# Performance work log

Hardware: AMD Instinct MI355X
Metric: run time of the kernel (lower is better)

The kernel has to match this reference:

```python
import jax, jax.numpy as jnp
import numpy as np

DX = 64  # state dim
DY = 64  # observation dim
B = 64   # batch of independent series
T = 512  # time_extent


def setup_inputs() -> dict:
    key = jax.random.key(0)
    ks = jax.random.split(key, 9)
    Ix = jnp.eye(DX, dtype=jnp.float32)
    Iy = jnp.eye(DY, dtype=jnp.float32)
    observation = jax.random.normal(ks[0], (T + 1, B, DY), dtype=jnp.float32)
    prior_mean = 0.1 * jax.random.normal(ks[1], (DX,), dtype=jnp.float32)
    prior_chol = 0.3 * Ix + jnp.tril(0.02 * jax.random.normal(ks[2], (DX, DX), dtype=jnp.float32))
    dynamic_weight = 0.9 * Ix + 0.02 * jax.random.normal(ks[3], (DX, DX), dtype=jnp.float32)
    dynamic_bias = 0.01 * jax.random.normal(ks[4], (DX,), dtype=jnp.float32)
    dynamic_chol = 0.3 * Ix + jnp.tril(0.02 * jax.random.normal(ks[5], (DX, DX), dtype=jnp.float32))
    observation_weight = Iy + 0.05 * jax.random.normal(ks[6], (DY, DX), dtype=jnp.float32)
    observation_bias = 0.01 * jax.random.normal(ks[7], (DY,), dtype=jnp.float32)
    observation_chol = 0.3 * Iy + jnp.tril(0.02 * jax.random.normal(ks[8], (DY, DY), dtype=jnp.float32))
    return {
        "time_extent": T,
        "observation": observation,
        "prior_mean": prior_mean,
        "prior_chol": prior_chol,
        "dynamic_weight": dynamic_weight,
        "dynamic_bias": dynamic_bias,
        "dynamic_chol": dynamic_chol,
        "observation_weight": observation_weight,
        "observation_bias": observation_bias,
        "observation_chol": observation_chol,
    }


def reference(time_extent, observation, prior_mean, prior_chol, dynamic_weight,
              dynamic_bias, dynamic_chol, observation_weight, observation_bias,
              observation_chol):
    dtype = observation.dtype
    dx = prior_mean.shape[-1]
    dy = observation.shape[-1]
    b = observation.shape[1]
    half_log_2pi = 0.5 * jnp.log(jnp.asarray(2.0 * np.pi, dtype))

    P0 = prior_chol @ prior_chol.T            # (dx, dx) prior covariance
    Q = dynamic_chol @ dynamic_chol.T         # process noise
    R = observation_chol @ observation_chol.T # observation noise
    F = dynamic_weight
    H = observation_weight
    Ix = jnp.eye(dx, dtype=dtype)

    def log_density(mean, cov, y):
        # mean: (1,dy) or (b,dy); cov: (dy,dy); y: (b,dy)
        res = y - mean
        inv = jnp.linalg.inv(cov)
        pref = -dy * half_log_2pi - 0.5 * jnp.linalg.slogdet(cov)[1]
        return pref - 0.5 * jnp.einsum('bi,ij,bj->b', res, inv, res)

    def bayes_update(mean, P, y):
        # mean: (b,dx) or (1,dx); P: (dx,dx); y: (b,dy)
        CW = P @ H.T                               # (dx, dy)
        S_inv = jnp.linalg.inv(H @ CW + R)         # (dy, dy)
        WIW = H.T @ S_inv @ H                      # (dx, dx)
        post_P = P @ (Ix - WIW @ P)
        post_mean = mean @ (Ix - P @ WIW).T + (y - observation_bias) @ (CW @ S_inv).T
        return post_mean, post_P

    # t = 0: predictive of observation from the prior
    obs_mean0 = prior_mean[None, :] @ H.T + observation_bias  # (1, dy)
    obs_cov0 = H @ P0 @ H.T + R
    ll0 = log_density(obs_mean0, obs_cov0, observation[0])
    m0, P0_post = bayes_update(prior_mean[None, :], P0, observation[0])
    m0 = jnp.broadcast_to(m0, (b, dx))

    def step(carry, y):
        m, P = carry
        pm = m @ F.T + dynamic_bias                # predictive mean (b, dx)
        pP = F @ P @ F.T + Q                       # predictive cov (dx, dx)
        om = pm @ H.T + observation_bias           # obs predictive mean
        oC = H @ pP @ H.T + R
        ll = log_density(om, oC, y)
        nm, nP = bayes_update(pm, pP, y)
        return (nm, nP), (nm, nP, ll)

    (_, _), (ms, Ps, lls) = jax.lax.scan(step, (m0, P0_post), observation[1:])
    posterior_means = jnp.concatenate([m0[None], ms], axis=0)          # (T+1, b, dx)
    covs = jnp.concatenate([P0_post[None], Ps], axis=0)                # (T+1, dx, dx)
    posterior_covariances = jnp.broadcast_to(covs[:, None], (time_extent + 1, b, dx, dx))
    likelihood_factors = jnp.concatenate([ll0[None], lls], axis=0)     # (T+1, b)
    return posterior_means, posterior_covariances, likelihood_factors
```

## Files before the change

kernel.cpp:

```cpp
#include <hip/hip_runtime.h>
#include <math.h>


#define TID ((int)threadIdx.x)
#define LDA 68
#define MAT 4096
#define BSLOT 4096
#define NSLOT 513
#define HEAD 64

#define WS_CSTAGE 0
#define WS_U      (NSLOT*MAT)
#define WS_EB     (WS_U + 9*MAT)
#define WS_CQ     (WS_EB + 4*MAT)
#define WS_CR     (WS_CQ + MAT)
#define WS_CHQ    (WS_CR + MAT)
#define WS_G      (WS_CHQ + MAT)
#define WS_KGT    (WS_G + MAT)
#define WS_HF     (WS_KGT + MAT)
#define WS_P0     (WS_HF + MAT)
#define WS_HP0    (WS_P0 + MAT)
#define WS_BA     (WS_HP0 + MAT)
#define WS_OBHDB  (WS_BA + 64)
#define WS_OM0    (WS_OBHDB + 64)
#define WS_HDB    (WS_OM0 + 64)
#define WS_SG     (WS_HDB + 64)
#define WS_B0     (WS_SG + MAT)
#define WS_B1     (WS_B0 + NSLOT*BSLOT)
#define WS_E0     (WS_B1 + NSLOT*BSLOT)
#define WS_E1     (WS_E0 + NSLOT*BSLOT)
#define WS_PP     (WS_E1 + NSLOT*BSLOT)
#define WS_SSI    (WS_PP + MAT)
#define WS_KST    (WS_SSI + MAT)
#define WS_BASS   (WS_KST + MAT)
#define WS_LDSS   (WS_BASS + 64)
#define WS_MK     (WS_LDSS + 64)

#define OUT_M 0
#define OUT_C 2101248
#define OUT_L 136581120

#define LLC (-58.81206612509905f)


__device__ __forceinline__ void tload(float* dst, const float* __restrict__ g) {
#pragma unroll
  for (int p = TID; p < 1024; p += 256) {
    int m = p >> 4, k4 = (p & 15) << 2;
    float4 v = *(const float4*)(g + m*64 + k4);
    dst[(k4+0)*LDA + m] = v.x;
    dst[(k4+1)*LDA + m] = v.y;
    dst[(k4+2)*LDA + m] = v.z;
    dst[(k4+3)*LDA + m] = v.w;
  }
}

__device__ __forceinline__ void tload_sub(float* dst, const float* __restrict__ g,
                                          const float* __restrict__ vec) {
#pragma unroll
  for (int p = TID; p < 1024; p += 256) {
    int m = p >> 4, k4 = (p & 15) << 2;
    float4 v = *(const float4*)(g + m*64 + k4);
    float4 s = *(const float4*)(vec + k4);
    dst[(k4+0)*LDA + m] = v.x - s.x;
    dst[(k4+1)*LDA + m] = v.y - s.y;
    dst[(k4+2)*LDA + m] = v.z - s.z;
    dst[(k4+3)*LDA + m] = v.w - s.w;
  }
}

__device__ __forceinline__ void pload(float* dst, const float* __restrict__ g) {
#pragma unroll
  for (int p = TID; p < 1024; p += 256) {
    int m = p >> 4, c4 = (p & 15) << 2;
    *(float4*)(dst + m*LDA + c4) = *(const float4*)(g + m*64 + c4);
  }
}

__device__ __forceinline__ void transcopy(float* dst, const float* src) {
#pragma unroll
  for (int p = TID; p < 1024; p += 256) {
    int m = p >> 4, k4 = (p & 15) << 2;
    float4 v = *(const float4*)(src + m*LDA + k4);
    dst[(k4+0)*LDA + m] = v.x;
    dst[(k4+1)*LDA + m] = v.y;
    dst[(k4+2)*LDA + m] = v.z;
    dst[(k4+3)*LDA + m] = v.w;
  }
}

__device__ __forceinline__ void gemm(const float* As, const float* Bs,
                                     float a[4][4], int tr, int tc) {
#pragma unroll
  for (int i = 0; i < 4; ++i)
#pragma unroll
    for (int j = 0; j < 4; ++j) a[i][j] = 0.f;
  const float* ap = As + (tr << 2);
  const float* bp = Bs + (tc << 2);
#pragma unroll 8
  for (int kk = 0; kk < 64; ++kk) {
    float4 av = *(const float4*)ap; ap += LDA;
    float4 bv = *(const float4*)bp; bp += LDA;
    a[0][0] = fmaf(av.x, bv.x, a[0][0]); a[0][1] = fmaf(av.x, bv.y, a[0][1]);
    a[0][2] = fmaf(av.x, bv.z, a[0][2]); a[0][3] = fmaf(av.x, bv.w, a[0][3]);
    a[1][0] = fmaf(av.y, bv.x, a[1][0]); a[1][1] = fmaf(av.y, bv.y, a[1][1]);
    a[1][2] = fmaf(av.y, bv.z, a[1][2]); a[1][3] = fmaf(av.y, bv.w, a[1][3]);
    a[2][0] = fmaf(av.z, bv.x, a[2][0]); a[2][1] = fmaf(av.z, bv.y, a[2][1]);
    a[2][2] = fmaf(av.z, bv.z, a[2][2]); a[2][3] = fmaf(av.z, bv.w, a[2][3]);
    a[3][0] = fmaf(av.w, bv.x, a[3][0]); a[3][1] = fmaf(av.w, bv.y, a[3][1]);
    a[3][2] = fmaf(av.w, bv.z, a[3][2]); a[3][3] = fmaf(av.w, bv.w, a[3][3]);
  }
}

__device__ __forceinline__ void add_g(float a[4][4], const float* __restrict__ g,
                                      int tr, int tc) {
#pragma unroll
  for (int i = 0; i < 4; ++i) {
    float4 v = *(const float4*)(g + (4*tr+i)*64 + 4*tc);
    a[i][0] += v.x; a[i][1] += v.y; a[i][2] += v.z; a[i][3] += v.w;
  }
}

__device__ __forceinline__ void rsub_g(float a[4][4], const float* __restrict__ g,
                                       int tr, int tc) {
#pragma unroll
  for (int i = 0; i < 4; ++i) {
    float4 v = *(const float4*)(g + (4*tr+i)*64 + 4*tc);
    a[i][0] = v.x - a[i][0]; a[i][1] = v.y - a[i][1];
    a[i][2] = v.z - a[i][2]; a[i][3] = v.w - a[i][3];
  }
}

__device__ __forceinline__ void addvec_g(float a[4][4], const float* __restrict__ v,
                                         int tc) {
  float4 s = *(const float4*)(v + 4*tc);
#pragma unroll
  for (int i = 0; i < 4; ++i) {
    a[i][0] += s.x; a[i][1] += s.y; a[i][2] += s.z; a[i][3] += s.w;
  }
}

__device__ __forceinline__ void addI(float a[4][4], int tr, int tc) {
  if (tr == tc) { a[0][0] += 1.f; a[1][1] += 1.f; a[2][2] += 1.f; a[3][3] += 1.f; }
}

__device__ __forceinline__ void gwrite(float* g, float a[4][4], int tr, int tc) {
#pragma unroll
  for (int i = 0; i < 4; ++i)
    *(float4*)(g + (4*tr+i)*64 + 4*tc) = make_float4(a[i][0], a[i][1], a[i][2], a[i][3]);
}

__device__ __forceinline__ void twrite_g(float* g, float a[4][4], int tr, int tc) {
#pragma unroll
  for (int i = 0; i < 4; ++i)
#pragma unroll
    for (int j = 0; j < 4; ++j)
      g[(4*tc+j)*64 + 4*tr+i] = a[i][j];
}

__device__ __forceinline__ void pstore(float* dst, float a[4][4], int tr, int tc) {
#pragma unroll
  for (int i = 0; i < 4; ++i)
    *(float4*)(dst + (4*tr+i)*LDA + 4*tc) = make_float4(a[i][0], a[i][1], a[i][2], a[i][3]);
}

__device__ __forceinline__ void tstore(float* dst, float a[4][4], int tr, int tc) {
#pragma unroll
  for (int i = 0; i < 4; ++i)
#pragma unroll
    for (int j = 0; j < 4; ++j)
      dst[(4*tc+j)*LDA + 4*tr+i] = a[i][j];
}

__device__ __forceinline__ void pwrite_g(float* g, const float* lds) {
#pragma unroll
  for (int p = TID; p < 1024; p += 256) {
    int m = p >> 4, c4 = (p & 15) << 2;
    *(float4*)(g + m*64 + c4) = *(const float4*)(lds + m*LDA + c4);
  }
}

__device__ float gj_inverse2(float* M, float* gjb, int wantLog) {
  const int i = TID >> 2, q = TID & 3;
  float r[16];
  {
    const float* base = M + i*LDA + 16*q;
    float4 v0 = *(const float4*)(base + 0);
    float4 v1 = *(const float4*)(base + 4);
    float4 v2 = *(const float4*)(base + 8);
    float4 v3 = *(const float4*)(base + 12);
    r[0]=v0.x; r[1]=v0.y; r[2]=v0.z; r[3]=v0.w;
    r[4]=v1.x; r[5]=v1.y; r[6]=v1.z; r[7]=v1.w;
    r[8]=v2.x; r[9]=v2.y; r[10]=v2.z; r[11]=v2.w;
    r[12]=v3.x; r[13]=v3.y; r[14]=v3.z; r[15]=v3.w;
  }
  float ld = 0.f;
  float* cb = gjb;
  float* rb = gjb + 128;
#pragma unroll 64
  for (int j = 0; j < 64; ++j) {
    float* cbp = cb + (j & 1) * 64;
    float* rbp = rb + (j & 1) * 64;
    if (q == (j >> 4)) cbp[i] = r[j & 15];
    if (i == j) {
      *(float4*)(rbp + 16*q + 0)  = make_float4(r[0], r[1], r[2], r[3]);
      *(float4*)(rbp + 16*q + 4)  = make_float4(r[4], r[5], r[6], r[7]);
      *(float4*)(rbp + 16*q + 8)  = make_float4(r[8], r[9], r[10], r[11]);
      *(float4*)(rbp + 16*q + 12) = make_float4(r[12], r[13], r[14], r[15]);
    }
    __syncthreads();
    float p = cbp[j];
    float rp = 1.0f / p;
    if (wantLog) ld += logf(p);
    float f = cbp[i];
    float mu = (i == j) ? (rp - 1.0f) : (0.0f - f * rp);
    float4 p0 = *(const float4*)(rbp + 16*q + 0);
    float4 p1 = *(const float4*)(rbp + 16*q + 4);
    float4 p2 = *(const float4*)(rbp + 16*q + 8);
    float4 p3 = *(const float4*)(rbp + 16*q + 12);
    r[0]  = fmaf(mu, p0.x, r[0]);  r[1]  = fmaf(mu, p0.y, r[1]);
    r[2]  = fmaf(mu, p0.z, r[2]);  r[3]  = fmaf(mu, p0.w, r[3]);
    r[4]  = fmaf(mu, p1.x, r[4]);  r[5]  = fmaf(mu, p1.y, r[5]);
    r[6]  = fmaf(mu, p1.z, r[6]);  r[7]  = fmaf(mu, p1.w, r[7]);
    r[8]  = fmaf(mu, p2.x, r[8]);  r[9]  = fmaf(mu, p2.y, r[9]);
    r[10] = fmaf(mu, p2.z, r[10]); r[11] = fmaf(mu, p2.w, r[11]);
    r[12] = fmaf(mu, p3.x, r[12]); r[13] = fmaf(mu, p3.y, r[13]);
    r[14] = fmaf(mu, p3.z, r[14]); r[15] = fmaf(mu, p3.w, r[15]);
    if (q == (j >> 4)) r[j & 15] = (i == j) ? rp : mu;
  }
  {
    float* base = M + i*LDA + 16*q;
    *(float4*)(base + 0)  = make_float4(r[0], r[1], r[2], r[3]);
    *(float4*)(base + 4)  = make_float4(r[4], r[5], r[6], r[7]);
    *(float4*)(base + 8)  = make_float4(r[8], r[9], r[10], r[11]);
    *(float4*)(base + 12) = make_float4(r[12], r[13], r[14], r[15]);
  }
  __syncthreads();
  return ld;
}

__device__ __forceinline__ int buf_parity(int s, int k) {
  if (s == 0) return 0;
  int li = 31 - __clz(s);
  int lu = li < (k - 1) ? li : (k - 1);
  return (lu + 1) & 1;
}

__device__ __forceinline__ float* bbuf(float* ws, int par) {
  return ws + (par ? WS_B1 : WS_B0);
}
__device__ __forceinline__ float* ebufp(float* ws, int par) {
  return ws + (par ? WS_E1 : WS_E0);
}

__device__ void prepA_body(int L, float* ws,
                           float* sA, float* sB, float* sT, float* sE,
                           float* gjb, int tr, int tc) {
  const float* AU = ws + WS_U + (size_t)(L % 3) * 3 * MAT;
  const float* CU = AU + MAT;
  const float* JU = AU + 2 * MAT;
  float* M2T = ws + WS_EB + (size_t)(L & 1) * 2 * MAT;
  float* EAo = M2T + MAT;
  float acc[4][4];

  pload(sA, CU); pload(sB, JU); __syncthreads();
  gemm(sA, sB, acc, tr, tc); addI(acc, tr, tc);
  __syncthreads(); pstore(sE, acc, tr, tc); __syncthreads();
  gj_inverse2(sE, gjb, 0);
  tload(sA, AU); __syncthreads();
  gemm(sA, sE, acc, tr, tc);
  twrite_g(M2T, acc, tr, tc);
  __syncthreads(); transcopy(sT, sE); pload(sB, AU); __syncthreads();
  gemm(sT, sB, acc, tr, tc);
  gwrite(EAo, acc, tr, tc);
}

__device__ void prepB1_body(int L, float* ws,
                            float* sA, float* sB, float* sT, float* sE,
                            float* gjb, int tr, int tc) {
  const float* AU = ws + WS_U + (size_t)(L % 3) * 3 * MAT;
  const float* CU = AU + MAT;
  const float* JU = AU + 2 * MAT;
  float* AUn = ws + WS_U + (size_t)((L + 1) % 3) * 3 * MAT;
  float* CUn = AUn + MAT;
  float acc[4][4];

  pload(sA, CU); pload(sB, JU); __syncthreads();
  gemm(sA, sB, acc, tr, tc); addI(acc, tr, tc);
  __syncthreads(); pstore(sE, acc, tr, tc); __syncthreads();
  gj_inverse2(sE, gjb, 0);
  tload(sB, AU); __syncthreads();
  gemm(sB, sE, acc, tr, tc);
  __syncthreads(); tstore(sT, acc, tr, tc); pload(sE, AU); __syncthreads();
  gemm(sT, sE, acc, tr, tc);
  gwrite(AUn, acc, tr, tc);
  gemm(sT, sA, acc, tr, tc);
  __syncthreads(); tstore(sE, acc, tr, tc); __syncthreads();
  gemm(sE, sB, acc, tr, tc);
  add_g(acc, CU, tr, tc); gwrite(CUn, acc, tr, tc);
}

__device__ void prepB2_body(int L, float* ws,
                            float* sA, float* sB, float* sT, float* sE,
                            float* gjb, int tr, int tc) {
  const float* AU = ws + WS_U + (size_t)(L % 3) * 3 * MAT;
  const float* CU = AU + MAT;
  const float* JU = AU + 2 * MAT;
  float* JUn = ws + WS_U + (size_t)((L + 1) % 3) * 3 * MAT + 2 * MAT;
  float acc[4][4];

  pload(sA, CU); pload(sB, JU); __syncthreads();
  gemm(sA, sB, acc, tr, tc); addI(acc, tr, tc);
  __syncthreads(); pstore(sE, acc, tr, tc); __syncthreads();
  gj_inverse2(sE, gjb, 0);
  gemm(sB, sE, acc, tr, tc);
  __syncthreads(); tstore(sT, acc, tr, tc); pload(sA, AU); __syncthreads();
  gemm(sT, sA, acc, tr, tc);
  __syncthreads(); pstore(sE, acc, tr, tc); __syncthreads();
  gemm(sA, sE, acc, tr, tc);
  add_g(acc, JU, tr, tc); gwrite(JUn, acc, tr, tc);
}

__device__ void bcast_body(const float* ws, float* out, int s) {
  const float4* src = (const float4*)(ws + WS_CSTAGE + (size_t)s * MAT);
  float4 c0 = src[TID], c1 = src[TID+256], c2 = src[TID+512], c3 = src[TID+768];
  float4* dst = (float4*)(out + OUT_C + (size_t)s * 64 * MAT);
  for (int bb = 0; bb < 64; ++bb) {
    float4* d = dst + (size_t)bb * 1024;
    d[TID] = c0; d[TID+256] = c1; d[TID+512] = c2; d[TID+768] = c3;
  }
}

__device__ void bcast_ss_body(const float* ws, float* out, int s) {
  const float4* src = (const float4*)(ws + WS_CSTAGE + (size_t)63 * MAT);
  float4 c0 = src[TID], c1 = src[TID+256], c2 = src[TID+512], c3 = src[TID+768];
  float4* dst = (float4*)(out + OUT_C + (size_t)s * 64 * MAT);
  for (int bb = 0; bb < 64; ++bb) {
    float4* d = dst + (size_t)bb * 1024;
    d[TID] = c0; d[TID+256] = c1; d[TID+512] = c2; d[TID+768] = c3;
  }
}

__device__ void ll_body(float* ws, float* out, const float* obs,
                        float* sA, float* sB, float* sT, float* sE,
                        float* gjb, int tr, int tc, int s) {
  int t = s + 1;
  const float* mp = out + OUT_M + (size_t)s * BSLOT;
  const float* Cp = ws + WS_CSTAGE + (size_t)s * MAT;
  float acc[4][4];

  tload(sA, ws + WS_HF); pload(sB, Cp); __syncthreads();
  gemm(sA, sB, acc, tr, tc);
  __syncthreads(); tstore(sT, acc, tr, tc); __syncthreads();
  gemm(sT, sA, acc, tr, tc);
  add_g(acc, ws + WS_SG, tr, tc);
  __syncthreads(); pstore(sE, acc, tr, tc); __syncthreads();
  float ldet = gj_inverse2(sE, gjb, 1);
  tload(sB, mp); __syncthreads();
  gemm(sB, sA, acc, tr, tc);
  addvec_g(acc, ws + WS_OBHDB, tc);
  const float* yt = obs + (size_t)t * BSLOT;
#pragma unroll
  for (int i2 = 0; i2 < 4; ++i2) {
    float4 v = *(const float4*)(yt + (4*tr+i2)*64 + 4*tc);
    acc[i2][0] = v.x - acc[i2][0]; acc[i2][1] = v.y - acc[i2][1];
    acc[i2][2] = v.z - acc[i2][2]; acc[i2][3] = v.w - acc[i2][3];
  }
  __syncthreads();
  pstore(sT, acc, tr, tc);
  tstore(sB, acc, tr, tc);
  __syncthreads();
  gemm(sB, sE, acc, tr, tc);
  __syncthreads(); pstore(sA, acc, tr, tc); __syncthreads();
  if (TID < 64) {
    float q = 0.f;
    for (int c = 0; c < 64; ++c) q = fmaf(sT[TID*LDA + c], sA[TID*LDA + c], q);
    out[OUT_L + (size_t)t * 64 + TID] = LLC - 0.5f * ldet - 0.5f * q;
  }
}

__device__ void ll_ss_body(float* ws, float* out, const float* obs,
                           float* sA, float* sB, float* sT, float* sE,
                           int tr, int tc, int t) {
  float acc[4][4];
  tload(sB, out + OUT_M + (size_t)(t - 1) * BSLOT);
  tload(sT, ws + WS_HF);
  pload(sE, ws + WS_SSI);
  __syncthreads();
  gemm(sB, sT, acc, tr, tc);
  addvec_g(acc, ws + WS_OBHDB, tc);
  const float* yt = obs + (size_t)t * BSLOT;
#pragma unroll
  for (int i2 = 0; i2 < 4; ++i2) {
    float4 v = *(const float4*)(yt + (4*tr+i2)*64 + 4*tc);
    acc[i2][0] = v.x - acc[i2][0]; acc[i2][1] = v.y - acc[i2][1];
    acc[i2][2] = v.z - acc[i2][2]; acc[i2][3] = v.w - acc[i2][3];
  }
  __syncthreads();
  pstore(sT, acc, tr, tc);
  tstore(sB, acc, tr, tc);
  __syncthreads();
  gemm(sB, sE, acc, tr, tc);
  __syncthreads(); pstore(sA, acc, tr, tc); __syncthreads();
  if (TID < 64) {
    float q = 0.f;
    for (int c = 0; c < 64; ++c) q = fmaf(sT[TID*LDA + c], sA[TID*LDA + c], q);
    out[OUT_L + (size_t)t * 64 + TID] = LLC - 0.5f * ws[WS_LDSS] - 0.5f * q;
  }
}

__global__ __launch_bounds__(256) void k_setup(
    float* ws, float* out, const float* obs, const float* pm, const float* pc,
    const float* F, const float* db, const float* dc, const float* H,
    const float* ob, const float* oc) {
  __shared__ __align__(16) float sA[64*LDA], sB[64*LDA], sT[64*LDA], sE[64*LDA];
  __shared__ __align__(16) float gjb[256];
  int tr = TID >> 4, tc = TID & 15;
  float acc[4][4];

  if (blockIdx.x == 0) {
    tload(sA, dc); __syncthreads();
    gemm(sA, sA, acc, tr, tc); gwrite(ws + WS_CQ, acc, tr, tc);
    __syncthreads();
    tload(sA, oc); __syncthreads();
    gemm(sA, sA, acc, tr, tc); gwrite(ws + WS_CR, acc, tr, tc);
    __syncthreads();
    tload(sA, H); pload(sB, ws + WS_CQ); __syncthreads();
    gemm(sA, sB, acc, tr, tc); gwrite(ws + WS_CHQ, acc, tr, tc);
    tstore(sT, acc, tr, tc);
    __syncthreads();
    gemm(sT, sA, acc, tr, tc); add_g(acc, ws + WS_CR, tr, tc);
    gwrite(ws + WS_SG, acc, tr, tc);
    __syncthreads(); pstore(sE, acc, tr, tc); __syncthreads();
    gj_inverse2(sE, gjb, 0);
    pload(sA, ws + WS_CHQ); __syncthreads();
    gemm(sA, sE, acc, tr, tc);
    twrite_g(ws + WS_KGT, acc, tr, tc);
    __syncthreads(); tstore(sT, acc, tr, tc); __syncthreads();
    tload(sA, H); pload(sB, F); __syncthreads();
    gemm(sA, sB, acc, tr, tc); gwrite(ws + WS_HF, acc, tr, tc);
    __syncthreads(); pstore(sB, acc, tr, tc); __syncthreads();
    gemm(sT, sB, acc, tr, tc); rsub_g(acc, F, tr, tc);
    gwrite(ws + WS_U + 0*MAT, acc, tr, tc);
    __syncthreads();
    pload(sB, ws + WS_CHQ); __syncthreads();
    gemm(sT, sB, acc, tr, tc); rsub_g(acc, ws + WS_CQ, tr, tc);
    gwrite(ws + WS_U + 1*MAT, acc, tr, tc);
    __syncthreads();
    pload(sB, ws + WS_HF); __syncthreads();
    gemm(sE, sB, acc, tr, tc);
    gwrite(ws + WS_G, acc, tr, tc);
    __syncthreads(); pstore(sT, acc, tr, tc); __syncthreads();
    gemm(sB, sT, acc, tr, tc);
    gwrite(ws + WS_U + 2*MAT, acc, tr, tc);
    __syncthreads();
    if (TID < 64) {
      float s = 0.f;
      for (int k = 0; k < 64; ++k) s = fmaf(H[TID*64 + k], db[k], s);
      ws[WS_HDB + TID] = s;
      ws[WS_OBHDB + TID] = s + ob[TID];
    }
    __syncthreads();
    if (TID < 64) {
      float s = 0.f;
      for (int k = 0; k < 64; ++k) s = fmaf(ws[WS_KGT + k*64 + TID], ws[WS_HDB + k], s);
      ws[WS_BA + TID] = db[TID] - s;
    }
  } else {
    float rt4[4][4];
    tload(sA, oc); __syncthreads();
    gemm(sA, sA, rt4, tr, tc);
    __syncthreads();
    tload(sA, pc); __syncthreads();
    gemm(sA, sA, acc, tr, tc);
    gwrite(ws + WS_P0, acc, tr, tc);
    __syncthreads(); pstore(sB, acc, tr, tc); __syncthreads();
    tload(sA, H); __syncthreads();
    gemm(sA, sB, acc, tr, tc);
    gwrite(ws + WS_HP0, acc, tr, tc);
    __syncthreads(); tstore(sT, acc, tr, tc); __syncthreads();
    gemm(sT, sA, acc, tr, tc);
#pragma unroll
    for (int i = 0; i < 4; ++i)
#pragma unroll
      for (int j = 0; j < 4; ++j) acc[i][j] += rt4[i][j];
    __syncthreads(); pstore(sE, acc, tr, tc); __syncthreads();
    float ldet = gj_inverse2(sE, gjb, 1);
    pload(sA, ws + WS_HP0); __syncthreads();
    gemm(sA, sE, acc, tr, tc);
    __syncthreads(); tstore(sT, acc, tr, tc); __syncthreads();
    pload(sB, ws + WS_HP0); __syncthreads();
    gemm(sT, sB, acc, tr, tc); rsub_g(acc, ws + WS_P0, tr, tc);
    gwrite(ws + WS_CSTAGE, acc, tr, tc);
    __syncthreads();
    if (TID < 64) {
      float s = 0.f;
      for (int k = 0; k < 64; ++k) s = fmaf(H[TID*64 + k], pm[k], s);
      ws[WS_OM0 + TID] = s + ob[TID];
    }
    __syncthreads();
    tload_sub(sA, obs, ws + WS_OM0); __syncthreads();
    gemm(sA, sT, acc, tr, tc); addvec_g(acc, pm, tc);
    gwrite(ws + WS_B0, acc, tr, tc);
    gwrite(out + OUT_M, acc, tr, tc);
    gemm(sA, sE, acc, tr, tc);
    __syncthreads(); pstore(sB, acc, tr, tc); __syncthreads();
    if (TID < 64) {
      float q = 0.f;
      for (int c = 0; c < 64; ++c) q = fmaf(sA[c*LDA + TID], sB[TID*LDA + c], q);
      out[OUT_L + TID] = LLC - 0.5f * ldet - 0.5f * q;
    }
    for (int idx = TID; idx < 4096; idx += 256) ws[WS_E0 + idx] = 0.f;
  }
}

__global__ __launch_bounds__(256) void k_init_head(
    float* ws, const float* obs, const float* ob) {
  __shared__ __align__(16) float sA[64*LDA], sB[64*LDA], sT[64*LDA], sE[64*LDA];
  __shared__ __align__(16) float gjb[256];
  int tr = TID >> 4, tc = TID & 15;
  int bid = blockIdx.x;
  if (bid >= 63) {
    if (bid == 63)      prepA_body(0, ws, sA, sB, sT, sE, gjb, tr, tc);
    else if (bid == 64) prepB1_body(0, ws, sA, sB, sT, sE, gjb, tr, tc);
    else                prepB2_body(0, ws, sA, sB, sT, sE, gjb, tr, tc);
    return;
  }
  int t = bid + 1;
  const float* yt = obs + (size_t)t * BSLOT;
  float acc[4][4];

  tload_sub(sA, yt, ob);
  pload(sB, ws + WS_KGT);
  __syncthreads();
  gemm(sA, sB, acc, tr, tc); addvec_g(acc, ws + WS_BA, tc);
  gwrite(ws + WS_B0 + (size_t)t * BSLOT, acc, tr, tc);
  __syncthreads();
  for (int idx = TID; idx < 4096; idx += 256) {
    int kk = idx >> 6, m = idx & 63;
    sA[kk*LDA + m] -= ws[WS_HDB + kk];
  }
  pload(sB, ws + WS_G);
  __syncthreads();
  gemm(sA, sB, acc, tr, tc);
  gwrite(ws + WS_E0 + (size_t)t * BSLOT, acc, tr, tc);
  (void)sT; (void)sE;
}

__global__ __launch_bounds__(256) void k_level_head(float* ws, float* out,
                                                    const float* obs, int k) {
  __shared__ __align__(16) float sA[64*LDA], sB[64*LDA], sT[64*LDA], sE[64*LDA];
  __shared__ __align__(16) float gjb[256];
  int tr = TID >> 4, tc = TID & 15;
  int bid = blockIdx.x;
  int nc = HEAD - (1 << k);

  if (bid < 3) {
    if (k <= 4) {
      if (bid == 0)      prepA_body(k + 1, ws, sA, sB, sT, sE, gjb, tr, tc);
      else if (bid == 1) prepB1_body(k + 1, ws, sA, sB, sT, sE, gjb, tr, tc);
      else               prepB2_body(k + 1, ws, sA, sB, sT, sE, gjb, tr, tc);
    }
    return;
  }
  if (bid >= 3 + nc) {
    int e = bid - (3 + nc);
    int ebase = k ? (1 << (k - 1)) : 0;
    int ecount = k ? (1 << (k - 1)) : 1;
    if (e < ecount) bcast_body(ws, out, ebase + e);
    else ll_body(ws, out, obs, sA, sB, sT, sE, gjb, tr, tc, ebase + (e - ecount));
    return;
  }

  int t = (1 << k) + bid - 3;
  int i = t - (1 << k);
  int pr = k & 1;
  int pw = (k + 1) & 1;
  int pl = buf_parity(i, k);
  const float* bi = bbuf(ws, pl) + (size_t)i * BSLOT;
  const float* ei = ebufp(ws, pl) + (size_t)i * BSLOT;
  const float* bj = bbuf(ws, pr) + (size_t)t * BSLOT;
  const float* ej = ebufp(ws, pr) + (size_t)t * BSLOT;
  float* bo = bbuf(ws, pw) + (size_t)t * BSLOT;
  float* eo = ebufp(ws, pw) + (size_t)t * BSLOT;
  const float* AU = ws + WS_U + (size_t)(k % 3) * 3 * MAT;
  const float* CU = AU + MAT;
  const float* JU = AU + 2 * MAT;
  const float* M2T = ws + WS_EB + (size_t)(k & 1) * 2 * MAT;
  const float* EAk = M2T + MAT;
  float acc[4][4];

  if (t >= (2 << k)) {
    tload(sA, ej); pload(sB, CU); __syncthreads();
    gemm(sA, sB, acc, tr, tc); add_g(acc, bi, tr, tc);
    tstore(sT, acc, tr, tc);
    __syncthreads();
    pload(sB, M2T); __syncthreads();
    gemm(sT, sB, acc, tr, tc); add_g(acc, bj, tr, tc);
    gwrite(bo, acc, tr, tc);
    __syncthreads();
    tload(sT, bi); pload(sB, JU); __syncthreads();
    gemm(sT, sB, acc, tr, tc);
#pragma unroll
    for (int i2 = 0; i2 < 4; ++i2)
#pragma unroll
      for (int j2 = 0; j2 < 4; ++j2) {
        int addr = (4*tc + j2)*LDA + 4*tr + i2;
        sA[addr] = sA[addr] - acc[i2][j2];
      }
    __syncthreads();
    pload(sB, EAk); __syncthreads();
    gemm(sA, sB, acc, tr, tc); add_g(acc, ei, tr, tc);
    gwrite(eo, acc, tr, tc);
  } else {
    const float* Ci = ws + WS_CSTAGE + (size_t)i * MAT;
    pload(sA, Ci); pload(sB, JU); __syncthreads();
    gemm(sA, sB, acc, tr, tc); addI(acc, tr, tc);
    __syncthreads(); pstore(sE, acc, tr, tc); __syncthreads();
    gj_inverse2(sE, gjb, 0);
    tload(sB, AU); __syncthreads();
    gemm(sB, sE, acc, tr, tc);
    __syncthreads(); tstore(sT, acc, tr, tc); __syncthreads();
    gemm(sT, sA, acc, tr, tc);
    __syncthreads(); tstore(sE, acc, tr, tc); __syncthreads();
    gemm(sE, sB, acc, tr, tc);
    add_g(acc, CU, tr, tc);
    gwrite(ws + WS_CSTAGE + (size_t)t * MAT, acc, tr, tc);
    __syncthreads();
    tload(sE, ej); __syncthreads();
    gemm(sE, sA, acc, tr, tc); add_g(acc, bi, tr, tc);
    __syncthreads(); tstore(sB, acc, tr, tc); __syncthreads();
    gemm(sB, sT, acc, tr, tc); add_g(acc, bj, tr, tc);
    gwrite(bo, acc, tr, tc);
    gwrite(out + OUT_M + (size_t)t * BSLOT, acc, tr, tc);
    (void)eo;
  }
}

__global__ __launch_bounds__(256) void k_ss(
    float* ws, float* out, const float* obs, const float* F, const float* H,
    const float* db) {
  __shared__ __align__(16) float sA[64*LDA], sB[64*LDA], sT[64*LDA], sE[64*LDA];
  __shared__ __align__(16) float gjb[256];
  int tr = TID >> 4, tc = TID & 15;
  int bid = blockIdx.x;

  if (bid == 64) {
    const float4* src = (const float4*)(out + OUT_M + (size_t)63 * BSLOT);
    float4* dst = (float4*)(ws + WS_B0);
#pragma unroll
    for (int q = 0; q < 4; ++q) dst[TID + 256*q] = src[TID + 256*q];
    return;
  }
  if (bid >= 32) { bcast_body(ws, out, bid); return; }
  if (bid >= 1) {
    ll_body(ws, out, obs, sA, sB, sT, sE, gjb, tr, tc, 31 + bid);
    return;
  }

  float acc[4][4];
  const float* C63 = ws + WS_CSTAGE + (size_t)63 * MAT;
  tload(sA, F); pload(sB, C63); __syncthreads();
  gemm(sA, sB, acc, tr, tc);
  __syncthreads(); tstore(sT, acc, tr, tc); __syncthreads();
  gemm(sT, sA, acc, tr, tc); add_g(acc, ws + WS_CQ, tr, tc);
  gwrite(ws + WS_PP, acc, tr, tc);
  __syncthreads(); pstore(sB, acc, tr, tc); __syncthreads();
  tload(sA, H); __syncthreads();
  gemm(sA, sB, acc, tr, tc);
  __syncthreads(); tstore(sT, acc, tr, tc); __syncthreads();
  gemm(sT, sA, acc, tr, tc); add_g(acc, ws + WS_CR, tr, tc);
  __syncthreads(); pstore(sE, acc, tr, tc); __syncthreads();
  float ldet = gj_inverse2(sE, gjb, 1);
  pwrite_g(ws + WS_SSI, sE);
  if (TID == 0) ws[WS_LDSS] = ldet;
  pload(sB, ws + WS_PP); __syncthreads();
  gemm(sB, sA, acc, tr, tc);
  __syncthreads(); tstore(sT, acc, tr, tc); __syncthreads();
  gemm(sT, sE, acc, tr, tc);
  twrite_g(ws + WS_KST, acc, tr, tc);
  __syncthreads(); tstore(sT, acc, tr, tc); __syncthreads();
  pload(sB, H); __syncthreads();
  gemm(sT, sB, acc, tr, tc);
  __syncthreads(); tstore(sT, acc, tr, tc); __syncthreads();
  if (TID < 64) {
    float s = 0.f;
    for (int kk = 0; kk < 64; ++kk) s = fmaf(sT[kk*LDA + TID], db[kk], s);
    ws[WS_BASS + TID] = db[TID] - s;
  }
  pload(sB, F); __syncthreads();
  gemm(sT, sB, acc, tr, tc); rsub_g(acc, F, tr, tc);
  twrite_g(ws + WS_MK, acc, tr, tc);
}

__global__ __launch_bounds__(256) void k_tail_init(
    float* ws, const float* obs, const float* ob) {
  __shared__ __align__(16) float sA[64*LDA], sB[64*LDA];
  int tr = TID >> 4, tc = TID & 15;
  int t = 64 + blockIdx.x;
  int i = t - 63;
  float acc[4][4];

  tload_sub(sA, obs + (size_t)t * BSLOT, ob);
  pload(sB, ws + WS_KST);
  __syncthreads();
  gemm(sA, sB, acc, tr, tc); addvec_g(acc, ws + WS_BASS, tc);
  gwrite(ws + WS_B0 + (size_t)i * BSLOT, acc, tr, tc);
}

__global__ __launch_bounds__(256) void k_tail_level(float* ws, float* out,
                                                    const float* obs, int k) {
  __shared__ __align__(16) float sA[64*LDA], sB[64*LDA], sT[64*LDA], sE[64*LDA];
  int tr = TID >> 4, tc = TID & 15;
  int bid = blockIdx.x;
  int ntc = 450 - (1 << k);
  float acc[4][4];

  if (bid == 0) {
    if (k <= 7) {
      const float* Mk = ws + WS_MK + (size_t)k * MAT;
      float* Mn = ws + WS_MK + (size_t)(k + 1) * MAT;
      tload(sA, Mk); pload(sB, Mk); __syncthreads();
      gemm(sA, sB, acc, tr, tc); gwrite(Mn, acc, tr, tc);
    }
    return;
  }
  if (bid < 1 + ntc) {
    int i = (1 << k) + bid - 1;
    int j = i - (1 << k);
    int pl = buf_parity(j, k);
    int pr = k & 1;
    int pw = (k + 1) & 1;
    const float* sj = bbuf(ws, pl) + (size_t)j * BSLOT;
    const float* si = bbuf(ws, pr) + (size_t)i * BSLOT;
    float* so = bbuf(ws, pw) + (size_t)i * BSLOT;
    tload(sA, sj); pload(sB, ws + WS_MK + (size_t)k * MAT); __syncthreads();
    gemm(sA, sB, acc, tr, tc); add_g(acc, si, tr, tc);
    gwrite(so, acc, tr, tc);
    if (i < (2 << k))
      gwrite(out + OUT_M + (size_t)(63 + i) * BSLOT, acc, tr, tc);
    return;
  }
  int e = bid - (1 + ntc);
  int nll = k ? (1 << (k - 1)) : 1;
  if (e < nll) {
    int t = k ? (64 + (1 << (k - 1)) + e) : 64;
    ll_ss_body(ws, out, obs, sA, sB, sT, sE, tr, tc, t);
    return;
  }
  int b = e - nll;
  bcast_ss_body(ws, out, 64 + 45 * k + b);
}

__global__ __launch_bounds__(256) void k_tail_final(float* ws, float* out,
                                                    const float* obs) {
  __shared__ __align__(16) float sA[64*LDA], sB[64*LDA], sT[64*LDA], sE[64*LDA];
  int tr = TID >> 4, tc = TID & 15;
  int bid = blockIdx.x;
  if (bid < 193) {
    ll_ss_body(ws, out, obs, sA, sB, sT, sE, tr, tc, 320 + bid);
  } else {
    bcast_ss_body(ws, out, 469 + (bid - 193));
  }
}

extern "C" void kernel_launch(void* const* d_in, const int* in_sizes, int n_in,
                              void* d_out, int out_size, void* d_ws, size_t ws_size,
                              hipStream_t stream) {
  (void)in_sizes; (void)n_in; (void)out_size; (void)ws_size;
  const float* obs = (const float*)d_in[1];
  const float* pm  = (const float*)d_in[2];
  const float* pc  = (const float*)d_in[3];
  const float* F   = (const float*)d_in[4];
  const float* db  = (const float*)d_in[5];
  const float* dc  = (const float*)d_in[6];
  const float* H   = (const float*)d_in[7];
  const float* ob  = (const float*)d_in[8];
  const float* oc  = (const float*)d_in[9];
  float* out = (float*)d_out;
  float* ws  = (float*)d_ws;

  k_setup<<<dim3(2), dim3(256), 0, stream>>>(ws, out, obs, pm, pc, F, db, dc, H, ob, oc);
  k_init_head<<<dim3(66), dim3(256), 0, stream>>>(ws, obs, ob);
  for (int k = 0; k <= 5; ++k) {
    int nc = HEAD - (1 << k);
    int ec = k ? (1 << (k - 1)) : 1;
    k_level_head<<<dim3(3 + nc + 2 * ec), dim3(256), 0, stream>>>(ws, out, obs, k);
  }
  k_ss<<<dim3(65), dim3(256), 0, stream>>>(ws, out, obs, F, H, db);
  k_tail_init<<<dim3(449), dim3(256), 0, stream>>>(ws, obs, ob);
  for (int k = 0; k <= 8; ++k) {
    int ntc = 450 - (1 << k);
    int nll = k ? (1 << (k - 1)) : 1;
    k_tail_level<<<dim3(1 + ntc + nll + 45), dim3(256), 0, stream>>>(ws, out, obs, k);
  }
  k_tail_final<<<dim3(237), dim3(256), 0, stream>>>(ws, out, obs);
}
```

Baseline: 1.126 ms.

## Fuse all launches into one persistent kernel with grid-wide atomic barriers

Replaces the sequence of about 20 kernel launches with a single persistent kernel of 450 blocks that runs each former launch as a phase, separated by a software grid barrier built on agent-scope atomics. The broadcast-of-steady-state-covariance work is also redistributed across phases to fill idle blocks. This removes per-launch overhead and launch gaps. In exchange it relies on all 450 blocks being co-resident (launch bounds of 2 blocks per CU), otherwise the barrier deadlocks, and it adds a memset plus spin-wait latency at every phase.

```diff
diff --git a/kernel.cpp b/kernel.cpp
--- a/kernel.cpp
+++ b/kernel.cpp
@@ -8,6 +8,7 @@
 #define BSLOT 4096
 #define NSLOT 513
 #define HEAD 64
+#define GRID 450
 
 #define WS_CSTAGE 0
 #define WS_U      (NSLOT*MAT)
@@ -35,12 +36,26 @@
 #define WS_BASS   (WS_KST + MAT)
 #define WS_LDSS   (WS_BASS + 64)
 #define WS_MK     (WS_LDSS + 64)
+#define WS_BAR    (WS_MK + 9*MAT)
 
 #define OUT_M 0
 #define OUT_C 2101248
 #define OUT_L 136581120
 
 #define LLC (-58.81206612509905f)
+
+__device__ __forceinline__ void gsync(unsigned* bar, int ph) {
+  __syncthreads();
+  if (TID == 0) {
+    __hip_atomic_fetch_add(&bar[ph], 1u, __ATOMIC_RELEASE,
+                           __HIP_MEMORY_SCOPE_AGENT);
+    while (__hip_atomic_load(&bar[ph], __ATOMIC_ACQUIRE,
+                             __HIP_MEMORY_SCOPE_AGENT) < (unsigned)gridDim.x) {
+      __builtin_amdgcn_s_sleep(2);
+    }
+  }
+  __syncthreads();
+}
 
 
 __device__ __forceinline__ void tload(float* dst, const float* __restrict__ g) {
@@ -409,127 +424,117 @@
   }
 }
 
-__global__ __launch_bounds__(256) void k_setup(
-    float* ws, float* out, const float* obs, const float* pm, const float* pc,
-    const float* F, const float* db, const float* dc, const float* H,
-    const float* ob, const float* oc) {
-  __shared__ __align__(16) float sA[64*LDA], sB[64*LDA], sT[64*LDA], sE[64*LDA];
-  __shared__ __align__(16) float gjb[256];
-  int tr = TID >> 4, tc = TID & 15;
-  float acc[4][4];
-
-  if (blockIdx.x == 0) {
-    tload(sA, dc); __syncthreads();
-    gemm(sA, sA, acc, tr, tc); gwrite(ws + WS_CQ, acc, tr, tc);
-    __syncthreads();
-    tload(sA, oc); __syncthreads();
-    gemm(sA, sA, acc, tr, tc); gwrite(ws + WS_CR, acc, tr, tc);
-    __syncthreads();
-    tload(sA, H); pload(sB, ws + WS_CQ); __syncthreads();
-    gemm(sA, sB, acc, tr, tc); gwrite(ws + WS_CHQ, acc, tr, tc);
-    tstore(sT, acc, tr, tc);
-    __syncthreads();
-    gemm(sT, sA, acc, tr, tc); add_g(acc, ws + WS_CR, tr, tc);
-    gwrite(ws + WS_SG, acc, tr, tc);
-    __syncthreads(); pstore(sE, acc, tr, tc); __syncthreads();
-    gj_inverse2(sE, gjb, 0);
-    pload(sA, ws + WS_CHQ); __syncthreads();
-    gemm(sA, sE, acc, tr, tc);
-    twrite_g(ws + WS_KGT, acc, tr, tc);
-    __syncthreads(); tstore(sT, acc, tr, tc); __syncthreads();
-    tload(sA, H); pload(sB, F); __syncthreads();
-    gemm(sA, sB, acc, tr, tc); gwrite(ws + WS_HF, acc, tr, tc);
-    __syncthreads(); pstore(sB, acc, tr, tc); __syncthreads();
-    gemm(sT, sB, acc, tr, tc); rsub_g(acc, F, tr, tc);
-    gwrite(ws + WS_U + 0*MAT, acc, tr, tc);
-    __syncthreads();
-    pload(sB, ws + WS_CHQ); __syncthreads();
-    gemm(sT, sB, acc, tr, tc); rsub_g(acc, ws + WS_CQ, tr, tc);
-    gwrite(ws + WS_U + 1*MAT, acc, tr, tc);
-    __syncthreads();
-    pload(sB, ws + WS_HF); __syncthreads();
-    gemm(sE, sB, acc, tr, tc);
-    gwrite(ws + WS_G, acc, tr, tc);
-    __syncthreads(); pstore(sT, acc, tr, tc); __syncthreads();
-    gemm(sB, sT, acc, tr, tc);
-    gwrite(ws + WS_U + 2*MAT, acc, tr, tc);
-    __syncthreads();
-    if (TID < 64) {
-      float s = 0.f;
-      for (int k = 0; k < 64; ++k) s = fmaf(H[TID*64 + k], db[k], s);
-      ws[WS_HDB + TID] = s;
-      ws[WS_OBHDB + TID] = s + ob[TID];
-    }
-    __syncthreads();
-    if (TID < 64) {
-      float s = 0.f;
-      for (int k = 0; k < 64; ++k) s = fmaf(ws[WS_KGT + k*64 + TID], ws[WS_HDB + k], s);
-      ws[WS_BA + TID] = db[TID] - s;
-    }
-  } else {
-    float rt4[4][4];
-    tload(sA, oc); __syncthreads();
-    gemm(sA, sA, rt4, tr, tc);
-    __syncthreads();
-    tload(sA, pc); __syncthreads();
-    gemm(sA, sA, acc, tr, tc);
-    gwrite(ws + WS_P0, acc, tr, tc);
-    __syncthreads(); pstore(sB, acc, tr, tc); __syncthreads();
-    tload(sA, H); __syncthreads();
-    gemm(sA, sB, acc, tr, tc);
-    gwrite(ws + WS_HP0, acc, tr, tc);
-    __syncthreads(); tstore(sT, acc, tr, tc); __syncthreads();
-    gemm(sT, sA, acc, tr, tc);
-#pragma unroll
-    for (int i = 0; i < 4; ++i)
-#pragma unroll
-      for (int j = 0; j < 4; ++j) acc[i][j] += rt4[i][j];
-    __syncthreads(); pstore(sE, acc, tr, tc); __syncthreads();
-    float ldet = gj_inverse2(sE, gjb, 1);
-    pload(sA, ws + WS_HP0); __syncthreads();
-    gemm(sA, sE, acc, tr, tc);
-    __syncthreads(); tstore(sT, acc, tr, tc); __syncthreads();
-    pload(sB, ws + WS_HP0); __syncthreads();
-    gemm(sT, sB, acc, tr, tc); rsub_g(acc, ws + WS_P0, tr, tc);
-    gwrite(ws + WS_CSTAGE, acc, tr, tc);
-    __syncthreads();
-    if (TID < 64) {
-      float s = 0.f;
-      for (int k = 0; k < 64; ++k) s = fmaf(H[TID*64 + k], pm[k], s);
-      ws[WS_OM0 + TID] = s + ob[TID];
-    }
-    __syncthreads();
-    tload_sub(sA, obs, ws + WS_OM0); __syncthreads();
-    gemm(sA, sT, acc, tr, tc); addvec_g(acc, pm, tc);
-    gwrite(ws + WS_B0, acc, tr, tc);
-    gwrite(out + OUT_M, acc, tr, tc);
-    gemm(sA, sE, acc, tr, tc);
-    __syncthreads(); pstore(sB, acc, tr, tc); __syncthreads();
-    if (TID < 64) {
-      float q = 0.f;
-      for (int c = 0; c < 64; ++c) q = fmaf(sA[c*LDA + TID], sB[TID*LDA + c], q);
-      out[OUT_L + TID] = LLC - 0.5f * ldet - 0.5f * q;
-    }
-    for (int idx = TID; idx < 4096; idx += 256) ws[WS_E0 + idx] = 0.f;
-  }
-}
-
-__global__ __launch_bounds__(256) void k_init_head(
-    float* ws, const float* obs, const float* ob) {
-  __shared__ __align__(16) float sA[64*LDA], sB[64*LDA], sT[64*LDA], sE[64*LDA];
-  __shared__ __align__(16) float gjb[256];
-  int tr = TID >> 4, tc = TID & 15;
-  int bid = blockIdx.x;
-  if (bid >= 63) {
-    if (bid == 63)      prepA_body(0, ws, sA, sB, sT, sE, gjb, tr, tc);
-    else if (bid == 64) prepB1_body(0, ws, sA, sB, sT, sE, gjb, tr, tc);
-    else                prepB2_body(0, ws, sA, sB, sT, sE, gjb, tr, tc);
-    return;
-  }
-  int t = bid + 1;
+__device__ void setup0_body(float* ws, const float* F, const float* db,
+                            const float* dc, const float* H, const float* ob,
+                            const float* oc,
+                            float* sA, float* sB, float* sT, float* sE,
+                            float* gjb, int tr, int tc) {
+  float acc[4][4];
+  tload(sA, dc); __syncthreads();
+  gemm(sA, sA, acc, tr, tc); gwrite(ws + WS_CQ, acc, tr, tc);
+  __syncthreads();
+  tload(sA, oc); __syncthreads();
+  gemm(sA, sA, acc, tr, tc); gwrite(ws + WS_CR, acc, tr, tc);
+  __syncthreads();
+  tload(sA, H); pload(sB, ws + WS_CQ); __syncthreads();
+  gemm(sA, sB, acc, tr, tc); gwrite(ws + WS_CHQ, acc, tr, tc);
+  tstore(sT, acc, tr, tc);
+  __syncthreads();
+  gemm(sT, sA, acc, tr, tc); add_g(acc, ws + WS_CR, tr, tc);
+  gwrite(ws + WS_SG, acc, tr, tc);
+  __syncthreads(); pstore(sE, acc, tr, tc); __syncthreads();
+  gj_inverse2(sE, gjb, 0);
+  pload(sA, ws + WS_CHQ); __syncthreads();
+  gemm(sA, sE, acc, tr, tc);
+  twrite_g(ws + WS_KGT, acc, tr, tc);
+  __syncthreads(); tstore(sT, acc, tr, tc); __syncthreads();
+  tload(sA, H); pload(sB, F); __syncthreads();
+  gemm(sA, sB, acc, tr, tc); gwrite(ws + WS_HF, acc, tr, tc);
+  __syncthreads(); pstore(sB, acc, tr, tc); __syncthreads();
+  gemm(sT, sB, acc, tr, tc); rsub_g(acc, F, tr, tc);
+  gwrite(ws + WS_U + 0*MAT, acc, tr, tc);
+  __syncthreads();
+  pload(sB, ws + WS_CHQ); __syncthreads();
+  gemm(sT, sB, acc, tr, tc); rsub_g(acc, ws + WS_CQ, tr, tc);
+  gwrite(ws + WS_U + 1*MAT, acc, tr, tc);
+  __syncthreads();
+  pload(sB, ws + WS_HF); __syncthreads();
+  gemm(sE, sB, acc, tr, tc);
+  gwrite(ws + WS_G, acc, tr, tc);
+  __syncthreads(); pstore(sT, acc, tr, tc); __syncthreads();
+  gemm(sB, sT, acc, tr, tc);
+  gwrite(ws + WS_U + 2*MAT, acc, tr, tc);
+  __syncthreads();
+  if (TID < 64) {
+    float s = 0.f;
+    for (int k = 0; k < 64; ++k) s = fmaf(H[TID*64 + k], db[k], s);
+    ws[WS_HDB + TID] = s;
+    ws[WS_OBHDB + TID] = s + ob[TID];
+  }
+  __syncthreads();
+  if (TID < 64) {
+    float s = 0.f;
+    for (int k = 0; k < 64; ++k) s = fmaf(ws[WS_KGT + k*64 + TID], ws[WS_HDB + k], s);
+    ws[WS_BA + TID] = db[TID] - s;
+  }
+}
+
+__device__ void setup1_full(float* ws, float* out, const float* obs,
+                            const float* pm, const float* pc, const float* H,
+                            const float* ob, const float* oc,
+                            float* sA, float* sB, float* sT, float* sE,
+                            float* gjb, int tr, int tc) {
+  float acc[4][4];
+  float rt4[4][4];
+  tload(sA, oc); __syncthreads();
+  gemm(sA, sA, rt4, tr, tc);
+  __syncthreads();
+  tload(sA, pc); __syncthreads();
+  gemm(sA, sA, acc, tr, tc);
+  gwrite(ws + WS_P0, acc, tr, tc);
+  __syncthreads(); pstore(sB, acc, tr, tc); __syncthreads();
+  tload(sA, H); __syncthreads();
+  gemm(sA, sB, acc, tr, tc);
+  gwrite(ws + WS_HP0, acc, tr, tc);
+  __syncthreads(); tstore(sT, acc, tr, tc); __syncthreads();
+  gemm(sT, sA, acc, tr, tc);
+#pragma unroll
+  for (int i = 0; i < 4; ++i)
+#pragma unroll
+    for (int j = 0; j < 4; ++j) acc[i][j] += rt4[i][j];
+  __syncthreads(); pstore(sE, acc, tr, tc); __syncthreads();
+  float ldet = gj_inverse2(sE, gjb, 1);
+  pload(sA, ws + WS_HP0); __syncthreads();
+  gemm(sA, sE, acc, tr, tc);
+  __syncthreads(); tstore(sT, acc, tr, tc); __syncthreads();
+  pload(sB, ws + WS_HP0); __syncthreads();
+  gemm(sT, sB, acc, tr, tc); rsub_g(acc, ws + WS_P0, tr, tc);
+  gwrite(ws + WS_CSTAGE, acc, tr, tc);
+  __syncthreads();
+  if (TID < 64) {
+    float s = 0.f;
+    for (int k = 0; k < 64; ++k) s = fmaf(H[TID*64 + k], pm[k], s);
+    ws[WS_OM0 + TID] = s + ob[TID];
+  }
+  __syncthreads();
+  tload_sub(sA, obs, ws + WS_OM0); __syncthreads();
+  gemm(sA, sT, acc, tr, tc); addvec_g(acc, pm, tc);
+  gwrite(ws + WS_B0, acc, tr, tc);
+  gwrite(out + OUT_M, acc, tr, tc);
+  gemm(sA, sE, acc, tr, tc);
+  __syncthreads(); pstore(sB, acc, tr, tc); __syncthreads();
+  if (TID < 64) {
+    float q = 0.f;
+    for (int c = 0; c < 64; ++c) q = fmaf(sA[c*LDA + TID], sB[TID*LDA + c], q);
+    out[OUT_L + TID] = LLC - 0.5f * ldet - 0.5f * q;
+  }
+  for (int idx = TID; idx < 4096; idx += 256) ws[WS_E0 + idx] = 0.f;
+}
+
+__device__ void initvec_body(float* ws, const float* obs, const float* ob,
+                             float* sA, float* sB, int tr, int tc, int t) {
   const float* yt = obs + (size_t)t * BSLOT;
   float acc[4][4];
-
   tload_sub(sA, yt, ob);
   pload(sB, ws + WS_KGT);
   __syncthreads();
@@ -544,16 +549,14 @@
   __syncthreads();
   gemm(sA, sB, acc, tr, tc);
   gwrite(ws + WS_E0 + (size_t)t * BSLOT, acc, tr, tc);
-  (void)sT; (void)sE;
-}
-
-__global__ __launch_bounds__(256) void k_level_head(float* ws, float* out,
-                                                    const float* obs, int k) {
-  __shared__ __align__(16) float sA[64*LDA], sB[64*LDA], sT[64*LDA], sE[64*LDA];
-  __shared__ __align__(16) float gjb[256];
-  int tr = TID >> 4, tc = TID & 15;
-  int bid = blockIdx.x;
+}
+
+__device__ void head_level_body(int k, int bid, float* ws, float* out,
+                                const float* obs,
+                                float* sA, float* sB, float* sT, float* sE,
+                                float* gjb, int tr, int tc) {
   int nc = HEAD - (1 << k);
+  int ec = k ? (1 << (k - 1)) : 1;
 
   if (bid < 3) {
     if (k <= 4) {
@@ -564,11 +567,12 @@
     return;
   }
   if (bid >= 3 + nc) {
-    int e = bid - (3 + nc);
-    int ebase = k ? (1 << (k - 1)) : 0;
-    int ecount = k ? (1 << (k - 1)) : 1;
-    if (e < ecount) bcast_body(ws, out, ebase + e);
-    else ll_body(ws, out, obs, sA, sB, sT, sE, gjb, tr, tc, ebase + (e - ecount));
+    if (bid < 3 + nc + 2 * ec) {
+      int e = bid - (3 + nc);
+      int ebase = k ? (1 << (k - 1)) : 0;
+      if (e < ec) bcast_body(ws, out, ebase + e);
+      else ll_body(ws, out, obs, sA, sB, sT, sE, gjb, tr, tc, ebase + (e - ec));
+    }
     return;
   }
 
@@ -637,27 +641,10 @@
   }
 }
 
-__global__ __launch_bounds__(256) void k_ss(
-    float* ws, float* out, const float* obs, const float* F, const float* H,
-    const float* db) {
-  __shared__ __align__(16) float sA[64*LDA], sB[64*LDA], sT[64*LDA], sE[64*LDA];
-  __shared__ __align__(16) float gjb[256];
-  int tr = TID >> 4, tc = TID & 15;
-  int bid = blockIdx.x;
-
-  if (bid == 64) {
-    const float4* src = (const float4*)(out + OUT_M + (size_t)63 * BSLOT);
-    float4* dst = (float4*)(ws + WS_B0);
-#pragma unroll
-    for (int q = 0; q < 4; ++q) dst[TID + 256*q] = src[TID + 256*q];
-    return;
-  }
-  if (bid >= 32) { bcast_body(ws, out, bid); return; }
-  if (bid >= 1) {
-    ll_body(ws, out, obs, sA, sB, sT, sE, gjb, tr, tc, 31 + bid);
-    return;
-  }
-
+__device__ void ss_chain_body(float* ws, const float* F, const float* H,
+                              const float* db,
+                              float* sA, float* sB, float* sT, float* sE,
+                              float* gjb, int tr, int tc) {
   float acc[4][4];
   const float* C63 = ws + WS_CSTAGE + (size_t)63 * MAT;
   tload(sA, F); pload(sB, C63); __syncthreads();
@@ -693,14 +680,11 @@
   twrite_g(ws + WS_MK, acc, tr, tc);
 }
 
-__global__ __launch_bounds__(256) void k_tail_init(
-    float* ws, const float* obs, const float* ob) {
-  __shared__ __align__(16) float sA[64*LDA], sB[64*LDA];
-  int tr = TID >> 4, tc = TID & 15;
-  int t = 64 + blockIdx.x;
-  int i = t - 63;
-  float acc[4][4];
-
+__device__ void tail_init_body(float* ws, const float* obs, const float* ob,
+                               float* sA, float* sB, int tr, int tc, int bid) {
+  int t = 64 + bid;
+  int i = bid + 1;
+  float acc[4][4];
   tload_sub(sA, obs + (size_t)t * BSLOT, ob);
   pload(sB, ws + WS_KST);
   __syncthreads();
@@ -708,24 +692,29 @@
   gwrite(ws + WS_B0 + (size_t)i * BSLOT, acc, tr, tc);
 }
 
-__global__ __launch_bounds__(256) void k_tail_level(float* ws, float* out,
-                                                    const float* obs, int k) {
-  __shared__ __align__(16) float sA[64*LDA], sB[64*LDA], sT[64*LDA], sE[64*LDA];
-  int tr = TID >> 4, tc = TID & 15;
-  int bid = blockIdx.x;
+__device__ void msq_body(int k, float* ws, float* sA, float* sB,
+                         int tr, int tc) {
+  const float* Mk = ws + WS_MK + (size_t)k * MAT;
+  float* Mn = ws + WS_MK + (size_t)(k + 1) * MAT;
+  float acc[4][4];
+  tload(sA, Mk); pload(sB, Mk); __syncthreads();
+  gemm(sA, sB, acc, tr, tc); gwrite(Mn, acc, tr, tc);
+  __syncthreads();
+}
+
+__device__ void tail_level_body(int k, int bid, float* ws, float* out,
+                                const float* obs,
+                                float* sA, float* sB, float* sT, float* sE,
+                                int tr, int tc) {
   int ntc = 450 - (1 << k);
   float acc[4][4];
 
   if (bid == 0) {
-    if (k <= 7) {
-      const float* Mk = ws + WS_MK + (size_t)k * MAT;
-      float* Mn = ws + WS_MK + (size_t)(k + 1) * MAT;
-      tload(sA, Mk); pload(sB, Mk); __syncthreads();
-      gemm(sA, sB, acc, tr, tc); gwrite(Mn, acc, tr, tc);
-    }
+    if (k <= 7) msq_body(k, ws, sA, sB, tr, tc);
+    if (k == 0) ll_ss_body(ws, out, obs, sA, sB, sT, sE, tr, tc, 64);
     return;
   }
-  if (bid < 1 + ntc) {
+  if (bid <= ntc) {
     int i = (1 << k) + bid - 1;
     int j = i - (1 << k);
     int pl = buf_parity(j, k);
@@ -741,26 +730,83 @@
       gwrite(out + OUT_M + (size_t)(63 + i) * BSLOT, acc, tr, tc);
     return;
   }
-  int e = bid - (1 + ntc);
-  int nll = k ? (1 << (k - 1)) : 1;
+  int e = bid - 1 - ntc;
+  int nll = (k >= 1) ? (1 << (k - 1)) : 0;
   if (e < nll) {
-    int t = k ? (64 + (1 << (k - 1)) + e) : 64;
-    ll_ss_body(ws, out, obs, sA, sB, sT, sE, tr, tc, t);
+    ll_ss_body(ws, out, obs, sA, sB, sT, sE, tr, tc, 64 + (1 << (k - 1)) + e);
     return;
   }
-  int b = e - nll;
-  bcast_ss_body(ws, out, 64 + 45 * k + b);
-}
-
-__global__ __launch_bounds__(256) void k_tail_final(float* ws, float* out,
-                                                    const float* obs) {
+  if (k >= 5) {
+    int b = e - nll;
+    int base, cnt;
+    if (k == 5)      { base = 264; cnt = 15; }
+    else if (k == 6) { base = 279; cnt = 31; }
+    else if (k == 7) { base = 310; cnt = 63; }
+    else             { base = 373; cnt = 127; }
+    if (b < cnt) bcast_ss_body(ws, out, base + b);
+  }
+}
+
+__device__ void phase_exec(int ph, int bid, float* ws, float* out,
+                           const float* obs, const float* pm, const float* pc,
+                           const float* F, const float* db, const float* dc,
+                           const float* H, const float* ob, const float* oc,
+                           float* sA, float* sB, float* sT, float* sE,
+                           float* gjb, int tr, int tc) {
+  if (ph == 0) {
+    if (bid == 0)
+      setup0_body(ws, F, db, dc, H, ob, oc, sA, sB, sT, sE, gjb, tr, tc);
+    else if (bid == 1)
+      setup1_full(ws, out, obs, pm, pc, H, ob, oc, sA, sB, sT, sE, gjb, tr, tc);
+  } else if (ph == 1) {
+    if (bid < 63)
+      initvec_body(ws, obs, ob, sA, sB, tr, tc, bid + 1);
+    else if (bid == 63) prepA_body(0, ws, sA, sB, sT, sE, gjb, tr, tc);
+    else if (bid == 64) prepB1_body(0, ws, sA, sB, sT, sE, gjb, tr, tc);
+    else if (bid == 65) prepB2_body(0, ws, sA, sB, sT, sE, gjb, tr, tc);
+  } else if (ph <= 7) {
+    head_level_body(ph - 2, bid, ws, out, obs, sA, sB, sT, sE, gjb, tr, tc);
+  } else if (ph == 8) {
+    if (bid == 0)
+      ss_chain_body(ws, F, H, db, sA, sB, sT, sE, gjb, tr, tc);
+    else if (bid < 32)
+      ll_body(ws, out, obs, sA, sB, sT, sE, gjb, tr, tc, 31 + bid);
+    else if (bid < 64)
+      bcast_body(ws, out, bid);
+    else if (bid == 64) {
+      const float4* src = (const float4*)(out + OUT_M + (size_t)63 * BSLOT);
+      float4* dst = (float4*)(ws + WS_B0);
+#pragma unroll
+      for (int q = 0; q < 4; ++q) dst[TID + 256*q] = src[TID + 256*q];
+    } else if (bid < 265)
+      bcast_ss_body(ws, out, 64 + (bid - 65));
+  } else if (ph == 9) {
+    if (bid < 449)
+      tail_init_body(ws, obs, ob, sA, sB, tr, tc, bid);
+  } else if (ph <= 18) {
+    tail_level_body(ph - 10, bid, ws, out, obs, sA, sB, sT, sE, tr, tc);
+  } else {
+    if (bid < 193)
+      ll_ss_body(ws, out, obs, sA, sB, sT, sE, tr, tc, 320 + bid);
+    else if (bid < 206)
+      bcast_ss_body(ws, out, 500 + (bid - 193));
+  }
+}
+
+__global__ __launch_bounds__(256, 2) void k_mega(
+    float* ws, float* out, const float* obs, const float* pm, const float* pc,
+    const float* F, const float* db, const float* dc, const float* H,
+    const float* ob, const float* oc) {
   __shared__ __align__(16) float sA[64*LDA], sB[64*LDA], sT[64*LDA], sE[64*LDA];
+  __shared__ __align__(16) float gjb[256];
   int tr = TID >> 4, tc = TID & 15;
   int bid = blockIdx.x;
-  if (bid < 193) {
-    ll_ss_body(ws, out, obs, sA, sB, sT, sE, tr, tc, 320 + bid);
-  } else {
-    bcast_ss_body(ws, out, 469 + (bid - 193));
+  unsigned* bar = (unsigned*)(ws + WS_BAR);
+
+  for (int ph = 0; ph < 20; ++ph) {
+    phase_exec(ph, bid, ws, out, obs, pm, pc, F, db, dc, H, ob, oc,
+               sA, sB, sT, sE, gjb, tr, tc);
+    if (ph < 19) gsync(bar, ph);
   }
 }
 
@@ -780,19 +826,7 @@
   float* out = (float*)d_out;
   float* ws  = (float*)d_ws;
 
-  k_setup<<<dim3(2), dim3(256), 0, stream>>>(ws, out, obs, pm, pc, F, db, dc, H, ob, oc);
-  k_init_head<<<dim3(66), dim3(256), 0, stream>>>(ws, obs, ob);
-  for (int k = 0; k <= 5; ++k) {
-    int nc = HEAD - (1 << k);
-    int ec = k ? (1 << (k - 1)) : 1;
-    k_level_head<<<dim3(3 + nc + 2 * ec), dim3(256), 0, stream>>>(ws, out, obs, k);
-  }
-  k_ss<<<dim3(65), dim3(256), 0, stream>>>(ws, out, obs, F, H, db);
-  k_tail_init<<<dim3(449), dim3(256), 0, stream>>>(ws, obs, ob);
-  for (int k = 0; k <= 8; ++k) {
-    int ntc = 450 - (1 << k);
-    int nll = k ? (1 << (k - 1)) : 1;
-    k_tail_level<<<dim3(1 + ntc + nll + 45), dim3(256), 0, stream>>>(ws, out, obs, k);
-  }
-  k_tail_final<<<dim3(237), dim3(256), 0, stream>>>(ws, out, obs);
-}
+  hipMemsetAsync((char*)d_ws + (size_t)WS_BAR * sizeof(float), 0, 128, stream);
+  k_mega<<<dim3(GRID), dim3(256), 0, stream>>>(
+      ws, out, obs, pm, pc, F, db, dc, H, ob, oc);
+}
```

Measured after the change: 3.198 ms. 2.84x slower.
